# Kernel optimization log

Hardware: AMD Instinct MI355X
Metric: run time of the kernel (lower is better)

## Reference

```python
import jax, jax.numpy as jnp
import numpy as np

B, S, D, H = 2, 2048, 1024, 16
HD = D // H  # head dim = 64


def setup_inputs() -> dict:
    key = jax.random.key(0)
    ks = jax.random.split(key, 8)
    s = 0.02
    return {
        "Q": jax.random.normal(ks[0], (B, S, D), jnp.float32),
        "K": jax.random.normal(ks[1], (B, S, D), jnp.float32),
        "V": jax.random.normal(ks[2], (B, S, D), jnp.float32),
        "mask": jax.random.randint(ks[3], (1, 1, S, S), 0, 2, jnp.int32),
        "Wq": jax.random.normal(ks[4], (D, D), jnp.float32) * s,
        "bq": jnp.zeros((D,), jnp.float32),
        "Wk": jax.random.normal(ks[5], (D, D), jnp.float32) * s,
        "bk": jnp.zeros((D,), jnp.float32),
        "Wv": jax.random.normal(ks[6], (D, D), jnp.float32) * s,
        "bv": jnp.zeros((D,), jnp.float32),
        "Wo": jax.random.normal(ks[7], (D, D), jnp.float32) * s,
        "bo": jnp.zeros((D,), jnp.float32),
    }


def reference(Q, K, V, mask, Wq, bq, Wk, bk, Wv, bv, Wo, bo):
    b = Q.shape[0]
    # QKV projections, split into heads: [B,S,D] -> [B,H,S,HD]
    q = (Q @ Wq + bq).reshape(b, -1, H, HD).transpose(0, 2, 1, 3)
    k = (K @ Wk + bk).reshape(b, -1, H, HD).transpose(0, 2, 1, 3)
    v = (V @ Wv + bv).reshape(b, -1, H, HD).transpose(0, 2, 1, 3)
    # scaled dot-product attention with full [B,H,S,S] scores (as in source)
    scale = jnp.sqrt(jnp.asarray(HD, q.dtype))
    scores = jnp.einsum("bhqd,bhkd->bhqk", q, k) / scale
    scores = jnp.where(mask == 0, -jnp.inf, scores)
    attn = jax.nn.softmax(scores, axis=-1)
    ctx = jnp.einsum("bhqk,bhkd->bhqd", attn, v)
    # merge heads and output projection
    concat = ctx.transpose(0, 2, 1, 3).reshape(b, -1, H * HD)
    return concat @ Wo + bo
```

## Files before the change

### kernel.cpp

```cpp
#include <hip/hip_runtime.h>


using s8v = __attribute__((ext_vector_type(8))) short;
using f4v = __attribute__((ext_vector_type(4))) float;
using f16v = __attribute__((ext_vector_type(16))) float;
typedef unsigned long long u64;

__device__ __forceinline__ unsigned short f2bf(float f) {
  union { float f; unsigned int u; } v; v.f = f;
  return (unsigned short)((v.u + 0x7fffu + ((v.u >> 16) & 1u)) >> 16);
}

__device__ __forceinline__ unsigned pkbf(float lo, float hi2) {
  return __builtin_amdgcn_perm(__float_as_uint(hi2), __float_as_uint(lo), 0x07060302);
}

__device__ __forceinline__ void gll16(const void* g, void* l) {
  __builtin_amdgcn_global_load_lds(
      (const __attribute__((address_space(1))) unsigned int*)g,
      (__attribute__((address_space(3))) unsigned int*)l, 16, 0, 0);
}

__global__ void prep_kernel(const float* __restrict__ Q, const float* __restrict__ K,
                            const float* __restrict__ V,
                            unsigned short* __restrict__ qb, unsigned short* __restrict__ kb,
                            unsigned short* __restrict__ vb,
                            const float* __restrict__ W0, const float* __restrict__ W1,
                            const float* __restrict__ W2, const float* __restrict__ W3,
                            unsigned short* __restrict__ T0, unsigned short* __restrict__ T1,
                            unsigned short* __restrict__ T2, unsigned short* __restrict__ T3,
                            const int* __restrict__ mask, unsigned* __restrict__ bmw) {
  __shared__ unsigned short t[64][72];
  const int bid = blockIdx.x, tid = threadIdx.x;
  if (bid < 12288) {
    int z = bid >> 12;
    int idx = (bid & 4095) * 256 + tid;
    const float* in = (z == 0) ? Q : (z == 1) ? K : V;
    unsigned short* out = (z == 0) ? qb : (z == 1) ? kb : vb;
    float4 v = ((const float4*)in)[idx];
    ushort4 o;
    o.x = f2bf(v.x); o.y = f2bf(v.y); o.z = f2bf(v.z); o.w = f2bf(v.w);
    ((ushort4*)out)[idx] = o;
  } else if (bid < 13312) {
    int b = bid - 12288;
    int z = b >> 8, rem = b & 255;
    int k0 = (rem >> 4) * 64, n0 = (rem & 15) * 64;
    const float* W = (z == 0) ? W0 : (z == 1) ? W1 : (z == 2) ? W2 : W3;
    unsigned short* Wt = (z == 0) ? T0 : (z == 1) ? T1 : (z == 2) ? T2 : T3;
    for (int p = 0; p < 4; ++p) {
      int idx = p * 256 + tid;
      int row = idx >> 4, c4 = idx & 15;
      float4 v = *(const float4*)&W[(size_t)(k0 + row) * 1024 + n0 + c4 * 4];
      t[row][c4 * 4 + 0] = f2bf(v.x);
      t[row][c4 * 4 + 1] = f2bf(v.y);
      t[row][c4 * 4 + 2] = f2bf(v.z);
      t[row][c4 * 4 + 3] = f2bf(v.w);
    }
    __syncthreads();
    for (int p = 0; p < 2; ++p) {
      int idx = p * 256 + tid;
      int j = idx >> 3, c8 = idx & 7;
      unsigned short tmp[8];
      for (int i = 0; i < 8; ++i) tmp[i] = t[c8 * 8 + i][j];
      uint4 o;
      o.x = tmp[0] | ((unsigned)tmp[1] << 16);
      o.y = tmp[2] | ((unsigned)tmp[3] << 16);
      o.z = tmp[4] | ((unsigned)tmp[5] << 16);
      o.w = tmp[6] | ((unsigned)tmp[7] << 16);
      *(uint4*)&Wt[(size_t)(n0 + j) * 1024 + k0 + c8 * 8] = o;
    }
  } else {
    int g = (bid - 13312) * 256 + tid;
    int widx = g & 15, hi = (g >> 4) & 1, l31 = (g >> 5) & 31;
    int it = (g >> 10) & 31, rowblk = g >> 15;
    int ni = widx >> 3, kcl = (widx >> 2) & 1, e = widx & 3;
    int kk = 64 * it + 32 * ni + 16 * kcl + 4 * hi + (e >> 1) * 8 + (e & 1) * 2;
    int qrow = rowblk * 32 + l31;
    const int* mrow = mask + (size_t)qrow * 2048 + kk;
    unsigned wd = (mrow[0] ? 0xFFFFu : 0u) | (mrow[1] ? 0xFFFF0000u : 0u);
    bmw[g] = wd;
  }
}

__global__ __launch_bounds__(256) void proj3_kernel(
    const unsigned short* __restrict__ A0, const unsigned short* __restrict__ A1,
    const unsigned short* __restrict__ A2,
    const unsigned short* __restrict__ W0, const unsigned short* __restrict__ W1,
    const unsigned short* __restrict__ W2,
    const float* __restrict__ b0, const float* __restrict__ b1, const float* __restrict__ b2,
    unsigned short* __restrict__ oq, unsigned short* __restrict__ ok,
    unsigned short* __restrict__ ovt) {
  const int z = blockIdx.z;
  const unsigned short* A  = (z == 0) ? A0 : (z == 1) ? A1 : A2;
  const unsigned short* Wt = (z == 0) ? W0 : (z == 1) ? W1 : W2;
  const float* bias        = (z == 0) ? b0 : (z == 1) ? b1 : b2;

  __shared__ __align__(16) unsigned short As[64 * 32];
  __shared__ __align__(16) unsigned short Bs[128 * 32];

  const int tid = threadIdx.x;
  const int lane = tid & 63, w = tid >> 6, ln = lane & 15, quad = lane >> 4;
  const int wm = (w & 1) * 32, wn = (w >> 1) * 64;
  const int m0 = blockIdx.x * 64, n0 = blockIdx.y * 128;

  const int slr = lane >> 2;
  const int schunk = (lane & 3) ^ ((lane >> 3) & 3);
  const int cfrag = (quad ^ ((ln >> 1) & 3)) * 8;

  f4v zero = {0.f, 0.f, 0.f, 0.f};
  f4v acc[2][4];
  for (int mi = 0; mi < 2; ++mi)
    for (int ni = 0; ni < 4; ++ni) acc[mi][ni] = zero;

  for (int kt = 0; kt < 1024; kt += 32) {
    __syncthreads();
    gll16(&A[(size_t)(m0 + w * 16 + slr) * 1024 + kt + schunk * 8],        &As[(w * 16) * 32]);
    gll16(&Wt[(size_t)(n0 + w * 32 + slr) * 1024 + kt + schunk * 8],       &Bs[(w * 32) * 32]);
    gll16(&Wt[(size_t)(n0 + w * 32 + 16 + slr) * 1024 + kt + schunk * 8],  &Bs[(w * 32 + 16) * 32]);
    __syncthreads();
    s8v a[2], b[4];
    for (int mi = 0; mi < 2; ++mi) a[mi] = *(const s8v*)&As[(wm + mi * 16 + ln) * 32 + cfrag];
    for (int ni = 0; ni < 4; ++ni) b[ni] = *(const s8v*)&Bs[(wn + ni * 16 + ln) * 32 + cfrag];
    if (z < 2) {
      for (int mi = 0; mi < 2; ++mi)
        for (int ni = 0; ni < 4; ++ni)
          acc[mi][ni] = __builtin_amdgcn_mfma_f32_16x16x32_bf16(a[mi], b[ni], acc[mi][ni], 0, 0, 0);
    } else {
      for (int mi = 0; mi < 2; ++mi)
        for (int ni = 0; ni < 4; ++ni)
          acc[mi][ni] = __builtin_amdgcn_mfma_f32_16x16x32_bf16(b[ni], a[mi], acc[mi][ni], 0, 0, 0);
    }
  }

  if (z < 2) {
    const float qscale = (z == 0) ? 0.18033688f : 1.0f;
    unsigned short* outp = (z == 0) ? oq : ok;
    for (int mi = 0; mi < 2; ++mi) {
      int rb = m0 + wm + mi * 16 + quad * 4;
      int b_ = rb >> 11;
      for (int ni = 0; ni < 4; ++ni) {
        int col = n0 + wn + ni * 16 + ln;
        float bvv = bias[col];
        int h = col >> 6, hd = col & 63;
        size_t ob = (size_t)(b_ * 16 + h) * 2048;
        for (int r = 0; r < 4; ++r) {
          int s = (rb + r) & 2047;
          outp[(ob + s) * 64 + hd] = f2bf((acc[mi][ni][r] + bvv) * qscale);
        }
      }
    }
  } else {
    for (int ni = 0; ni < 4; ++ni) {
      for (int r = 0; r < 4; ++r) {
        int colw = n0 + wn + ni * 16 + quad * 4 + r;
        int h = colw >> 6, hd = colw & 63;
        float bvv = bias[colw];
        for (int mi = 0; mi < 2; ++mi) {
          int sg = m0 + wm + mi * 16 + ln;
          int b_ = sg >> 11, ss = sg & 2047;
          ovt[((size_t)(b_ * 16 + h) * 64 + hd) * 2048 + ss] = f2bf(acc[mi][ni][r] + bvv);
        }
      }
    }
  }
}

__global__ __launch_bounds__(256, 2) void flash_kernel(
    const unsigned short* __restrict__ q, const unsigned short* __restrict__ k,
    const unsigned short* __restrict__ vt, const unsigned* __restrict__ bmw,
    unsigned short* __restrict__ ctx) {
  __shared__ __align__(16) unsigned short k_s[2][64][72];
  __shared__ __align__(16) unsigned short v_s[2][64][72];

  const int tid = threadIdx.x;
  const int lane = tid & 63, w = tid >> 6;
  const int l31 = lane & 31, hi = lane >> 5;
  const int q0 = blockIdx.x * 128;
  const int bh = blockIdx.y;
  const unsigned short* qg  = q  + ((size_t)bh * 2048 + q0) * 64;
  const unsigned short* kgb = k  + (size_t)bh * 2048 * 64;
  const unsigned short* vgb = vt + (size_t)bh * 64 * 2048;
  const unsigned* mwp = bmw + (size_t)(blockIdx.x * 4 + w) * 32768 + l31 * 32 + hi * 16;

  const int qrow = w * 32 + l31;
  s8v qf[4];
#pragma unroll
  for (int c = 0; c < 4; ++c)
    qf[c] = *(const s8v*)&qg[(size_t)qrow * 64 + c * 16 + hi * 8];

  s8v ones;
#pragma unroll
  for (int i = 0; i < 8; ++i) ones[i] = (short)0x3F80;
  f16v zf;
#pragma unroll
  for (int i = 0; i < 16; ++i) zf[i] = 0.f;

  const int srow = tid >> 3, sc8 = tid & 7;

  uint4 kr0 = *(const uint4*)&kgb[(size_t)srow * 64 + sc8 * 8];
  uint4 kr1 = *(const uint4*)&kgb[(size_t)(srow + 32) * 64 + sc8 * 8];
  uint4 vr0 = *(const uint4*)&vgb[(size_t)srow * 2048 + sc8 * 8];
  uint4 vr1 = *(const uint4*)&vgb[(size_t)(srow + 32) * 2048 + sc8 * 8];
  *(uint4*)&k_s[0][srow][sc8 * 8] = kr0;
  *(uint4*)&k_s[0][srow + 32][sc8 * 8] = kr1;
  *(uint4*)&v_s[0][srow][sc8 * 8] = vr0;
  *(uint4*)&v_s[0][srow + 32][sc8 * 8] = vr1;
  kr0 = *(const uint4*)&kgb[(size_t)(64 + srow) * 64 + sc8 * 8];
  kr1 = *(const uint4*)&kgb[(size_t)(64 + srow + 32) * 64 + sc8 * 8];
  vr0 = *(const uint4*)&vgb[(size_t)srow * 2048 + 64 + sc8 * 8];
  vr1 = *(const uint4*)&vgb[(size_t)(srow + 32) * 2048 + 64 + sc8 * 8];
  __syncthreads();

  f16v o0, o1, lac;
#pragma unroll
  for (int i = 0; i < 16; ++i) { o0[i] = 0.f; o1[i] = 0.f; lac[i] = 0.f; }

  for (int kt = 0; kt < 2048; kt += 64) {
    const int cur = (kt >> 6) & 1;
    const uint4* mw4 = (const uint4*)(mwp + (kt >> 6) * 1024);
    const uint4 mwA = mw4[0], mwB = mw4[1], mwC = mw4[2], mwD = mw4[3];

    if (kt + 64 < 2048) {
      const int nxt = cur ^ 1;
      *(uint4*)&k_s[nxt][srow][sc8 * 8] = kr0;
      *(uint4*)&k_s[nxt][srow + 32][sc8 * 8] = kr1;
      *(uint4*)&v_s[nxt][srow][sc8 * 8] = vr0;
      *(uint4*)&v_s[nxt][srow + 32][sc8 * 8] = vr1;
      if (kt + 128 < 2048) {
        const int kn = kt + 128;
        kr0 = *(const uint4*)&kgb[(size_t)(kn + srow) * 64 + sc8 * 8];
        kr1 = *(const uint4*)&kgb[(size_t)(kn + srow + 32) * 64 + sc8 * 8];
        vr0 = *(const uint4*)&vgb[(size_t)srow * 2048 + kn + sc8 * 8];
        vr1 = *(const uint4*)&vgb[(size_t)(srow + 32) * 2048 + kn + sc8 * 8];
      }
    }

    __builtin_amdgcn_s_setprio(1);
    s8v ak0 = *(const s8v*)&k_s[cur][l31][hi * 8];
    s8v ak1 = *(const s8v*)&k_s[cur][32 + l31][hi * 8];
    f16v s0 = __builtin_amdgcn_mfma_f32_32x32x16_bf16(ak0, qf[0], zf, 0, 0, 0);
    f16v s1 = __builtin_amdgcn_mfma_f32_32x32x16_bf16(ak1, qf[0], zf, 0, 0, 0);
#pragma unroll
    for (int c = 1; c < 4; ++c) {
      ak0 = *(const s8v*)&k_s[cur][l31][c * 16 + hi * 8];
      ak1 = *(const s8v*)&k_s[cur][32 + l31][c * 16 + hi * 8];
      s0 = __builtin_amdgcn_mfma_f32_32x32x16_bf16(ak0, qf[c], s0, 0, 0, 0);
      s1 = __builtin_amdgcn_mfma_f32_32x32x16_bf16(ak1, qf[c], s1, 0, 0, 0);
    }
    __builtin_amdgcn_s_setprio(0);

    s8v pf[4];
#pragma unroll
    for (int ni = 0; ni < 2; ++ni) {
      float p[16];
#pragma unroll
      for (int i = 0; i < 16; ++i)
        p[i] = __builtin_amdgcn_exp2f(ni ? s1[i] : s0[i]);
#pragma unroll
      for (int kcl = 0; kcl < 2; ++kcl) {
        const int rb = 8 * kcl;
        const uint4 mw = ni ? (kcl ? mwD : mwC) : (kcl ? mwB : mwA);
        unsigned x0 = pkbf(p[rb + 0], p[rb + 1]) & mw.x;
        unsigned x1 = pkbf(p[rb + 2], p[rb + 3]) & mw.y;
        unsigned y0 = pkbf(p[rb + 4], p[rb + 5]) & mw.z;
        unsigned y1 = pkbf(p[rb + 6], p[rb + 7]) & mw.w;
        asm("v_permlane32_swap_b32 %0, %1" : "+v"(x0), "+v"(y0));
        asm("v_permlane32_swap_b32 %0, %1" : "+v"(x1), "+v"(y1));
        union { uint4 u; s8v v; } cv;
        cv.u = make_uint4(x0, x1, y0, y1);
        pf[ni * 2 + kcl] = cv.v;
      }
    }

    __builtin_amdgcn_s_setprio(1);
#pragma unroll
    for (int kc = 0; kc < 4; ++kc)
      lac = __builtin_amdgcn_mfma_f32_32x32x16_bf16(pf[kc], ones, lac, 0, 0, 0);
#pragma unroll
    for (int kc = 0; kc < 4; ++kc) {
      s8v bv0 = *(const s8v*)&v_s[cur][l31][kc * 16 + hi * 8];
      s8v bv1 = *(const s8v*)&v_s[cur][32 + l31][kc * 16 + hi * 8];
      o0 = __builtin_amdgcn_mfma_f32_32x32x16_bf16(pf[kc], bv0, o0, 0, 0, 0);
      o1 = __builtin_amdgcn_mfma_f32_32x32x16_bf16(pf[kc], bv1, o1, 0, 0, 0);
    }
    __builtin_amdgcn_s_setprio(0);
    __syncthreads();
  }

  const int b_ = bh >> 4, h = bh & 15;
#pragma unroll
  for (int r = 0; r < 16; ++r) {
    const int ql = (r & 3) + 8 * (r >> 2) + 4 * hi;
    const float inv = 1.f / lac[r];
    const int srw = q0 + w * 32 + ql;
    const size_t base = ((size_t)b_ * 2048 + srw) * 1024 + h * 64;
    ctx[base + l31] = f2bf(o0[r] * inv);
    ctx[base + 32 + l31] = f2bf(o1[r] * inv);
  }
}

__global__ __launch_bounds__(256) void gemm_out_kernel(
    const unsigned short* __restrict__ A, const unsigned short* __restrict__ Wt,
    const float* __restrict__ bias, float* __restrict__ out) {
  __shared__ __align__(16) unsigned short As[64 * 32];
  __shared__ __align__(16) unsigned short Bs[128 * 32];

  const int tid = threadIdx.x;
  const int lane = tid & 63, w = tid >> 6, ln = lane & 15, quad = lane >> 4;
  const int wm = (w & 1) * 32, wn = (w >> 1) * 64;
  const int m0 = blockIdx.x * 64, n0 = blockIdx.y * 128;

  const int slr = lane >> 2;
  const int schunk = (lane & 3) ^ ((lane >> 3) & 3);
  const int cfrag = (quad ^ ((ln >> 1) & 3)) * 8;

  f4v zero = {0.f, 0.f, 0.f, 0.f};
  f4v acc[2][4];
  for (int mi = 0; mi < 2; ++mi)
    for (int ni = 0; ni < 4; ++ni) acc[mi][ni] = zero;

  for (int kt = 0; kt < 1024; kt += 32) {
    __syncthreads();
    gll16(&A[(size_t)(m0 + w * 16 + slr) * 1024 + kt + schunk * 8],        &As[(w * 16) * 32]);
    gll16(&Wt[(size_t)(n0 + w * 32 + slr) * 1024 + kt + schunk * 8],       &Bs[(w * 32) * 32]);
    gll16(&Wt[(size_t)(n0 + w * 32 + 16 + slr) * 1024 + kt + schunk * 8],  &Bs[(w * 32 + 16) * 32]);
    __syncthreads();
    s8v a[2], b[4];
    for (int mi = 0; mi < 2; ++mi) a[mi] = *(const s8v*)&As[(wm + mi * 16 + ln) * 32 + cfrag];
    for (int ni = 0; ni < 4; ++ni) b[ni] = *(const s8v*)&Bs[(wn + ni * 16 + ln) * 32 + cfrag];
    for (int mi = 0; mi < 2; ++mi)
      for (int ni = 0; ni < 4; ++ni)
        acc[mi][ni] = __builtin_amdgcn_mfma_f32_16x16x32_bf16(a[mi], b[ni], acc[mi][ni], 0, 0, 0);
  }

  for (int mi = 0; mi < 2; ++mi) {
    int rb = m0 + wm + mi * 16 + quad * 4;
    for (int ni = 0; ni < 4; ++ni) {
      int col = n0 + wn + ni * 16 + ln;
      float bvv = bias[col];
      for (int r = 0; r < 4; ++r)
        out[(size_t)(rb + r) * 1024 + col] = acc[mi][ni][r] + bvv;
    }
  }
}

extern "C" void kernel_launch(void* const* d_in, const int* in_sizes, int n_in,
                              void* d_out, int out_size, void* d_ws, size_t ws_size,
                              hipStream_t stream) {
  const float* Q  = (const float*)d_in[0];
  const float* K  = (const float*)d_in[1];
  const float* V  = (const float*)d_in[2];
  const int* mask = (const int*)d_in[3];
  const float* Wq = (const float*)d_in[4];
  const float* bq = (const float*)d_in[5];
  const float* Wk = (const float*)d_in[6];
  const float* bk = (const float*)d_in[7];
  const float* Wv = (const float*)d_in[8];
  const float* bv = (const float*)d_in[9];
  const float* Wo = (const float*)d_in[10];
  const float* bo = (const float*)d_in[11];
  float* out = (float*)d_out;

  char* ws = (char*)d_ws;
  const size_t MB = 1u << 20;
  unsigned short* qb  = (unsigned short*)(ws + 0 * MB);
  unsigned short* kb  = (unsigned short*)(ws + 8 * MB);
  unsigned short* vb  = (unsigned short*)(ws + 16 * MB);
  unsigned short* wqt = (unsigned short*)(ws + 24 * MB);
  unsigned short* wkt = (unsigned short*)(ws + 26 * MB);
  unsigned short* wvt = (unsigned short*)(ws + 28 * MB);
  unsigned short* wot = (unsigned short*)(ws + 30 * MB);
  unsigned short* qh  = (unsigned short*)(ws + 32 * MB);
  unsigned short* kh  = (unsigned short*)(ws + 40 * MB);
  unsigned short* vth = (unsigned short*)(ws + 48 * MB);
  unsigned* bmw       = (unsigned*)(ws + 56 * MB);
  unsigned short* ctx = (unsigned short*)(ws + 16 * MB);

  prep_kernel<<<21504, 256, 0, stream>>>(Q, K, V, qb, kb, vb,
                                         Wq, Wk, Wv, Wo, wqt, wkt, wvt, wot,
                                         mask, bmw);
  proj3_kernel<<<dim3(64, 8, 3), 256, 0, stream>>>(qb, kb, vb, wqt, wkt, wvt,
                                                   bq, bk, bv, qh, kh, vth);
  flash_kernel<<<dim3(16, 32), 256, 0, stream>>>(qh, kh, vth, bmw, ctx);
  gemm_out_kernel<<<dim3(64, 8), 256, 0, stream>>>(ctx, wot, bo, out);
}
```

Measured before the change: 247.3 us.

## Split flash attention KV range across warp pairs with 64-row query blocks

Each flash block now handles 64 query rows instead of 128. Its four waves form two groups, and each group processes half of the key range, one taking the first 1024 keys and the other the last 1024, using both LDS buffers at the same time. The partial outputs and row sums are combined through shared memory before normalisation. The grid doubles to 1024 blocks and the launch bounds ask for 3 blocks per CU, to improve occupancy and load balance across the GPU's CUs. In exchange, the double-buffer overlap now needs two barriers per iteration and there is an extra reduction step at the end.

New measurement: 265.2 us. +7.2%, slower.

```diff
diff --git a/kernel.cpp b/kernel.cpp
--- a/kernel.cpp
+++ b/kernel.cpp
@@ -165,7 +165,7 @@
   }
 }
 
-__global__ __launch_bounds__(256, 2) void flash_kernel(
+__global__ __launch_bounds__(256, 3) void flash_kernel(
     const unsigned short* __restrict__ q, const unsigned short* __restrict__ k,
     const unsigned short* __restrict__ vt, const unsigned* __restrict__ bmw,
     unsigned short* __restrict__ ctx) {
@@ -175,14 +175,17 @@
   const int tid = threadIdx.x;
   const int lane = tid & 63, w = tid >> 6;
   const int l31 = lane & 31, hi = lane >> 5;
-  const int q0 = blockIdx.x * 128;
+  const int h = w & 1;
+  const int g = w >> 1;
+  const int q0 = blockIdx.x * 64;
   const int bh = blockIdx.y;
   const unsigned short* qg  = q  + ((size_t)bh * 2048 + q0) * 64;
   const unsigned short* kgb = k  + (size_t)bh * 2048 * 64;
   const unsigned short* vgb = vt + (size_t)bh * 64 * 2048;
-  const unsigned* mwp = bmw + (size_t)(blockIdx.x * 4 + w) * 32768 + l31 * 32 + hi * 16;
-
-  const int qrow = w * 32 + l31;
+  const unsigned* mwp = bmw + ((size_t)(blockIdx.x * 2 + g) * 32 + h * 16) * 1024
+                        + l31 * 32 + hi * 16;
+
+  const int qrow = g * 32 + l31;
   s8v qf[4];
 #pragma unroll
   for (int c = 0; c < 4; ++c)
@@ -197,53 +200,51 @@
 
   const int srow = tid >> 3, sc8 = tid & 7;
 
-  uint4 kr0 = *(const uint4*)&kgb[(size_t)srow * 64 + sc8 * 8];
-  uint4 kr1 = *(const uint4*)&kgb[(size_t)(srow + 32) * 64 + sc8 * 8];
-  uint4 vr0 = *(const uint4*)&vgb[(size_t)srow * 2048 + sc8 * 8];
-  uint4 vr1 = *(const uint4*)&vgb[(size_t)(srow + 32) * 2048 + sc8 * 8];
-  *(uint4*)&k_s[0][srow][sc8 * 8] = kr0;
-  *(uint4*)&k_s[0][srow + 32][sc8 * 8] = kr1;
-  *(uint4*)&v_s[0][srow][sc8 * 8] = vr0;
-  *(uint4*)&v_s[0][srow + 32][sc8 * 8] = vr1;
-  kr0 = *(const uint4*)&kgb[(size_t)(64 + srow) * 64 + sc8 * 8];
-  kr1 = *(const uint4*)&kgb[(size_t)(64 + srow + 32) * 64 + sc8 * 8];
-  vr0 = *(const uint4*)&vgb[(size_t)srow * 2048 + 64 + sc8 * 8];
-  vr1 = *(const uint4*)&vgb[(size_t)(srow + 32) * 2048 + 64 + sc8 * 8];
+  uint4 ka0, ka1, kb0, kb1, va0, va1, vb0, vb1;
+  auto LOADT = [&](int it) {
+    const int kA = it * 64, kB = 1024 + it * 64;
+    ka0 = *(const uint4*)&kgb[(size_t)(kA + srow) * 64 + sc8 * 8];
+    ka1 = *(const uint4*)&kgb[(size_t)(kA + srow + 32) * 64 + sc8 * 8];
+    kb0 = *(const uint4*)&kgb[(size_t)(kB + srow) * 64 + sc8 * 8];
+    kb1 = *(const uint4*)&kgb[(size_t)(kB + srow + 32) * 64 + sc8 * 8];
+    va0 = *(const uint4*)&vgb[(size_t)srow * 2048 + kA + sc8 * 8];
+    va1 = *(const uint4*)&vgb[(size_t)(srow + 32) * 2048 + kA + sc8 * 8];
+    vb0 = *(const uint4*)&vgb[(size_t)srow * 2048 + kB + sc8 * 8];
+    vb1 = *(const uint4*)&vgb[(size_t)(srow + 32) * 2048 + kB + sc8 * 8];
+  };
+  auto WRITET = [&]() {
+    *(uint4*)&k_s[0][srow][sc8 * 8] = ka0;
+    *(uint4*)&k_s[0][srow + 32][sc8 * 8] = ka1;
+    *(uint4*)&k_s[1][srow][sc8 * 8] = kb0;
+    *(uint4*)&k_s[1][srow + 32][sc8 * 8] = kb1;
+    *(uint4*)&v_s[0][srow][sc8 * 8] = va0;
+    *(uint4*)&v_s[0][srow + 32][sc8 * 8] = va1;
+    *(uint4*)&v_s[1][srow][sc8 * 8] = vb0;
+    *(uint4*)&v_s[1][srow + 32][sc8 * 8] = vb1;
+  };
+
+  LOADT(0);
+  WRITET();
+  LOADT(1);
   __syncthreads();
 
   f16v o0, o1, lac;
 #pragma unroll
   for (int i = 0; i < 16; ++i) { o0[i] = 0.f; o1[i] = 0.f; lac[i] = 0.f; }
 
-  for (int kt = 0; kt < 2048; kt += 64) {
-    const int cur = (kt >> 6) & 1;
-    const uint4* mw4 = (const uint4*)(mwp + (kt >> 6) * 1024);
+  for (int i = 0; i < 16; ++i) {
+    const uint4* mw4 = (const uint4*)(mwp + i * 1024);
     const uint4 mwA = mw4[0], mwB = mw4[1], mwC = mw4[2], mwD = mw4[3];
 
-    if (kt + 64 < 2048) {
-      const int nxt = cur ^ 1;
-      *(uint4*)&k_s[nxt][srow][sc8 * 8] = kr0;
-      *(uint4*)&k_s[nxt][srow + 32][sc8 * 8] = kr1;
-      *(uint4*)&v_s[nxt][srow][sc8 * 8] = vr0;
-      *(uint4*)&v_s[nxt][srow + 32][sc8 * 8] = vr1;
-      if (kt + 128 < 2048) {
-        const int kn = kt + 128;
-        kr0 = *(const uint4*)&kgb[(size_t)(kn + srow) * 64 + sc8 * 8];
-        kr1 = *(const uint4*)&kgb[(size_t)(kn + srow + 32) * 64 + sc8 * 8];
-        vr0 = *(const uint4*)&vgb[(size_t)srow * 2048 + kn + sc8 * 8];
-        vr1 = *(const uint4*)&vgb[(size_t)(srow + 32) * 2048 + kn + sc8 * 8];
-      }
-    }
-
     __builtin_amdgcn_s_setprio(1);
-    s8v ak0 = *(const s8v*)&k_s[cur][l31][hi * 8];
-    s8v ak1 = *(const s8v*)&k_s[cur][32 + l31][hi * 8];
+    s8v ak0 = *(const s8v*)&k_s[h][l31][hi * 8];
+    s8v ak1 = *(const s8v*)&k_s[h][32 + l31][hi * 8];
     f16v s0 = __builtin_amdgcn_mfma_f32_32x32x16_bf16(ak0, qf[0], zf, 0, 0, 0);
     f16v s1 = __builtin_amdgcn_mfma_f32_32x32x16_bf16(ak1, qf[0], zf, 0, 0, 0);
 #pragma unroll
     for (int c = 1; c < 4; ++c) {
-      ak0 = *(const s8v*)&k_s[cur][l31][c * 16 + hi * 8];
-      ak1 = *(const s8v*)&k_s[cur][32 + l31][c * 16 + hi * 8];
+      ak0 = *(const s8v*)&k_s[h][l31][c * 16 + hi * 8];
+      ak1 = *(const s8v*)&k_s[h][32 + l31][c * 16 + hi * 8];
       s0 = __builtin_amdgcn_mfma_f32_32x32x16_bf16(ak0, qf[c], s0, 0, 0, 0);
       s1 = __builtin_amdgcn_mfma_f32_32x32x16_bf16(ak1, qf[c], s1, 0, 0, 0);
     }
@@ -254,8 +255,8 @@
     for (int ni = 0; ni < 2; ++ni) {
       float p[16];
 #pragma unroll
-      for (int i = 0; i < 16; ++i)
-        p[i] = __builtin_amdgcn_exp2f(ni ? s1[i] : s0[i]);
+      for (int i2 = 0; i2 < 16; ++i2)
+        p[i2] = __builtin_amdgcn_exp2f(ni ? s1[i2] : s0[i2]);
 #pragma unroll
       for (int kcl = 0; kcl < 2; ++kcl) {
         const int rb = 8 * kcl;
@@ -278,24 +279,43 @@
       lac = __builtin_amdgcn_mfma_f32_32x32x16_bf16(pf[kc], ones, lac, 0, 0, 0);
 #pragma unroll
     for (int kc = 0; kc < 4; ++kc) {
-      s8v bv0 = *(const s8v*)&v_s[cur][l31][kc * 16 + hi * 8];
-      s8v bv1 = *(const s8v*)&v_s[cur][32 + l31][kc * 16 + hi * 8];
+      s8v bv0 = *(const s8v*)&v_s[h][l31][kc * 16 + hi * 8];
+      s8v bv1 = *(const s8v*)&v_s[h][32 + l31][kc * 16 + hi * 8];
       o0 = __builtin_amdgcn_mfma_f32_32x32x16_bf16(pf[kc], bv0, o0, 0, 0, 0);
       o1 = __builtin_amdgcn_mfma_f32_32x32x16_bf16(pf[kc], bv1, o1, 0, 0, 0);
     }
     __builtin_amdgcn_s_setprio(0);
-    __syncthreads();
-  }
-
-  const int b_ = bh >> 4, h = bh & 15;
-#pragma unroll
-  for (int r = 0; r < 16; ++r) {
-    const int ql = (r & 3) + 8 * (r >> 2) + 4 * hi;
-    const float inv = 1.f / lac[r];
-    const int srw = q0 + w * 32 + ql;
-    const size_t base = ((size_t)b_ * 2048 + srw) * 1024 + h * 64;
-    ctx[base + l31] = f2bf(o0[r] * inv);
-    ctx[base + 32 + l31] = f2bf(o1[r] * inv);
+
+    __syncthreads();
+    if (i < 15) WRITET();
+    if (i < 14) LOADT(i + 2);
+    __syncthreads();
+  }
+
+  float* cb = g ? (float*)&v_s[0][0][0] : (float*)&k_s[0][0][0];
+  if (h == 1) {
+#pragma unroll
+    for (int r = 0; r < 16; r += 4) {
+      *(float4*)&cb[lane * 52 + r]      = make_float4(o0[r], o0[r+1], o0[r+2], o0[r+3]);
+      *(float4*)&cb[lane * 52 + 16 + r] = make_float4(o1[r], o1[r+1], o1[r+2], o1[r+3]);
+      *(float4*)&cb[lane * 52 + 32 + r] = make_float4(lac[r], lac[r+1], lac[r+2], lac[r+3]);
+    }
+  }
+  __syncthreads();
+  if (h == 0) {
+    const int b_ = bh >> 4, hh = bh & 15;
+#pragma unroll
+    for (int r = 0; r < 16; ++r) {
+      const float oo0 = o0[r] + cb[lane * 52 + r];
+      const float oo1 = o1[r] + cb[lane * 52 + 16 + r];
+      const float ll  = lac[r] + cb[lane * 52 + 32 + r];
+      const float inv = 1.f / ll;
+      const int ql = (r & 3) + 8 * (r >> 2) + 4 * hi;
+      const int srw = q0 + g * 32 + ql;
+      const size_t base = ((size_t)b_ * 2048 + srw) * 1024 + hh * 64;
+      ctx[base + l31] = f2bf(oo0 * inv);
+      ctx[base + 32 + l31] = f2bf(oo1 * inv);
+    }
   }
 }
 
@@ -381,6 +401,6 @@
                                          mask, bmw);
   proj3_kernel<<<dim3(64, 8, 3), 256, 0, stream>>>(qb, kb, vb, wqt, wkt, wvt,
                                                    bq, bk, bv, qh, kh, vth);
-  flash_kernel<<<dim3(16, 32), 256, 0, stream>>>(qh, kh, vth, bmw, ctx);
+  flash_kernel<<<dim3(32, 32), 256, 0, stream>>>(qh, kh, vth, bmw, ctx);
   gemm_out_kernel<<<dim3(64, 8), 256, 0, stream>>>(ctx, wot, bo, out);
 }
```

## Software-pipeline QK^T of the next tile with softmax and PV of the current

Applied to the files above, without the earlier changes.

Restructures the flash attention loop so the QK^T MFMAs for tile i+1 are issued before the exp/pack and PV MFMAs of tile i, with the score registers ping-ponged through a two-way manually unrolled macro. This lets matrix-core work overlap the exp and permute VALU work. The mask words for the next tile are prefetched one iteration ahead, and the global-to-LDS staging is rescheduled with two barriers per iteration. It raises register pressure with two live score sets, which may hurt occupancy under launch_bounds(256,2).

New measurement: 246.1 us. About the same (-0.5%).

```diff
diff --git a/kernel.cpp b/kernel.cpp
--- a/kernel.cpp
+++ b/kernel.cpp
@@ -165,6 +165,74 @@
   }
 }
 
+#define FLASH_ITER(i, SIN0, SIN1, SOUT0, SOUT1)                                 \
+  {                                                                             \
+    const int cur = (i) & 1;                                                    \
+    uint4 nA, nB, nC, nD;                                                       \
+    if ((i) < 31) {                                                             \
+      const uint4* m4 = (const uint4*)(mwp + ((i) + 1) * 1024);                 \
+      nA = m4[0]; nB = m4[1]; nC = m4[2]; nD = m4[3];                           \
+    }                                                                           \
+          \
+    __builtin_amdgcn_s_setprio(1);                                              \
+    if ((i) < 31) {                                                             \
+      s8v ak0 = *(const s8v*)&k_s[cur ^ 1][l31][hi * 8];                        \
+      s8v ak1 = *(const s8v*)&k_s[cur ^ 1][32 + l31][hi * 8];                   \
+      SOUT0 = __builtin_amdgcn_mfma_f32_32x32x16_bf16(ak0, qf[0], zf, 0, 0, 0); \
+      SOUT1 = __builtin_amdgcn_mfma_f32_32x32x16_bf16(ak1, qf[0], zf, 0, 0, 0); \
+      _Pragma("unroll")                                                         \
+      for (int c = 1; c < 4; ++c) {                                             \
+        ak0 = *(const s8v*)&k_s[cur ^ 1][l31][c * 16 + hi * 8];                 \
+        ak1 = *(const s8v*)&k_s[cur ^ 1][32 + l31][c * 16 + hi * 8];            \
+        SOUT0 = __builtin_amdgcn_mfma_f32_32x32x16_bf16(ak0, qf[c], SOUT0, 0, 0, 0); \
+        SOUT1 = __builtin_amdgcn_mfma_f32_32x32x16_bf16(ak1, qf[c], SOUT1, 0, 0, 0); \
+      }                                                                         \
+    }                                                                           \
+    __builtin_amdgcn_s_setprio(0);                                              \
+         \
+    s8v pf[4];                                                                  \
+    _Pragma("unroll")                                                           \
+    for (int ni = 0; ni < 2; ++ni) {                                            \
+      const f16v sv = ni ? SIN1 : SIN0;                                         \
+      _Pragma("unroll")                                                         \
+      for (int kcl = 0; kcl < 2; ++kcl) {                                       \
+        const int rb = 8 * kcl;                                                 \
+        const uint4 mw = ni ? (kcl ? mwD : mwC) : (kcl ? mwB : mwA);            \
+        unsigned x0 = pkbf(__builtin_amdgcn_exp2f(sv[rb + 0]),                  \
+                           __builtin_amdgcn_exp2f(sv[rb + 1])) & mw.x;          \
+        unsigned x1 = pkbf(__builtin_amdgcn_exp2f(sv[rb + 2]),                  \
+                           __builtin_amdgcn_exp2f(sv[rb + 3])) & mw.y;          \
+        unsigned y0 = pkbf(__builtin_amdgcn_exp2f(sv[rb + 4]),                  \
+                           __builtin_amdgcn_exp2f(sv[rb + 5])) & mw.z;          \
+        unsigned y1 = pkbf(__builtin_amdgcn_exp2f(sv[rb + 6]),                  \
+                           __builtin_amdgcn_exp2f(sv[rb + 7])) & mw.w;          \
+        asm("v_permlane32_swap_b32 %0, %1" : "+v"(x0), "+v"(y0));               \
+        asm("v_permlane32_swap_b32 %0, %1" : "+v"(x1), "+v"(y1));               \
+        union { uint4 u; s8v v; } cv;                                           \
+        cv.u = make_uint4(x0, x1, y0, y1);                                      \
+        pf[ni * 2 + kcl] = cv.v;                                                \
+      }                                                                         \
+    }                                                                           \
+                                              \
+    __builtin_amdgcn_s_setprio(1);                                              \
+    _Pragma("unroll")                                                           \
+    for (int kc = 0; kc < 4; ++kc)                                              \
+      lac = __builtin_amdgcn_mfma_f32_32x32x16_bf16(pf[kc], ones, lac, 0, 0, 0);\
+    _Pragma("unroll")                                                           \
+    for (int kc = 0; kc < 4; ++kc) {                                            \
+      s8v bv0 = *(const s8v*)&v_s[cur][l31][kc * 16 + hi * 8];                  \
+      s8v bv1 = *(const s8v*)&v_s[cur][32 + l31][kc * 16 + hi * 8];             \
+      o0 = __builtin_amdgcn_mfma_f32_32x32x16_bf16(pf[kc], bv0, o0, 0, 0, 0);   \
+      o1 = __builtin_amdgcn_mfma_f32_32x32x16_bf16(pf[kc], bv1, o1, 0, 0, 0);   \
+    }                                                                           \
+    __builtin_amdgcn_s_setprio(0);                                              \
+    __syncthreads();                             \
+    if ((i) < 30) WRITET(cur);                         \
+    if ((i) < 29) LOADT((i) + 3);                                               \
+    __syncthreads();                      \
+    mwA = nA; mwB = nB; mwC = nC; mwD = nD;                                     \
+  }
+
 __global__ __launch_bounds__(256, 2) void flash_kernel(
     const unsigned short* __restrict__ q, const unsigned short* __restrict__ k,
     const unsigned short* __restrict__ vt, const unsigned* __restrict__ bmw,
@@ -197,94 +265,55 @@
 
   const int srow = tid >> 3, sc8 = tid & 7;
 
-  uint4 kr0 = *(const uint4*)&kgb[(size_t)srow * 64 + sc8 * 8];
-  uint4 kr1 = *(const uint4*)&kgb[(size_t)(srow + 32) * 64 + sc8 * 8];
-  uint4 vr0 = *(const uint4*)&vgb[(size_t)srow * 2048 + sc8 * 8];
-  uint4 vr1 = *(const uint4*)&vgb[(size_t)(srow + 32) * 2048 + sc8 * 8];
-  *(uint4*)&k_s[0][srow][sc8 * 8] = kr0;
-  *(uint4*)&k_s[0][srow + 32][sc8 * 8] = kr1;
-  *(uint4*)&v_s[0][srow][sc8 * 8] = vr0;
-  *(uint4*)&v_s[0][srow + 32][sc8 * 8] = vr1;
-  kr0 = *(const uint4*)&kgb[(size_t)(64 + srow) * 64 + sc8 * 8];
-  kr1 = *(const uint4*)&kgb[(size_t)(64 + srow + 32) * 64 + sc8 * 8];
-  vr0 = *(const uint4*)&vgb[(size_t)srow * 2048 + 64 + sc8 * 8];
-  vr1 = *(const uint4*)&vgb[(size_t)(srow + 32) * 2048 + 64 + sc8 * 8];
+  uint4 kr0, kr1, vr0, vr1;
+  auto LOADT = [&](int it) {
+    const int kk = it * 64;
+    kr0 = *(const uint4*)&kgb[(size_t)(kk + srow) * 64 + sc8 * 8];
+    kr1 = *(const uint4*)&kgb[(size_t)(kk + srow + 32) * 64 + sc8 * 8];
+    vr0 = *(const uint4*)&vgb[(size_t)srow * 2048 + kk + sc8 * 8];
+    vr1 = *(const uint4*)&vgb[(size_t)(srow + 32) * 2048 + kk + sc8 * 8];
+  };
+  auto WRITET = [&](int b) {
+    *(uint4*)&k_s[b][srow][sc8 * 8] = kr0;
+    *(uint4*)&k_s[b][srow + 32][sc8 * 8] = kr1;
+    *(uint4*)&v_s[b][srow][sc8 * 8] = vr0;
+    *(uint4*)&v_s[b][srow + 32][sc8 * 8] = vr1;
+  };
+
+  LOADT(0); WRITET(0);
+  LOADT(1); WRITET(1);
+  LOADT(2);
   __syncthreads();
 
+  uint4 mwA, mwB, mwC, mwD;
+  {
+    const uint4* m4 = (const uint4*)mwp;
+    mwA = m4[0]; mwB = m4[1]; mwC = m4[2]; mwD = m4[3];
+  }
+
+  f16v sA0, sA1, sB0, sB1;
+  {
+    s8v ak0 = *(const s8v*)&k_s[0][l31][hi * 8];
+    s8v ak1 = *(const s8v*)&k_s[0][32 + l31][hi * 8];
+    sA0 = __builtin_amdgcn_mfma_f32_32x32x16_bf16(ak0, qf[0], zf, 0, 0, 0);
+    sA1 = __builtin_amdgcn_mfma_f32_32x32x16_bf16(ak1, qf[0], zf, 0, 0, 0);
+#pragma unroll
+    for (int c = 1; c < 4; ++c) {
+      ak0 = *(const s8v*)&k_s[0][l31][c * 16 + hi * 8];
+      ak1 = *(const s8v*)&k_s[0][32 + l31][c * 16 + hi * 8];
+      sA0 = __builtin_amdgcn_mfma_f32_32x32x16_bf16(ak0, qf[c], sA0, 0, 0, 0);
+      sA1 = __builtin_amdgcn_mfma_f32_32x32x16_bf16(ak1, qf[c], sA1, 0, 0, 0);
+    }
+  }
+
   f16v o0, o1, lac;
 #pragma unroll
   for (int i = 0; i < 16; ++i) { o0[i] = 0.f; o1[i] = 0.f; lac[i] = 0.f; }
 
-  for (int kt = 0; kt < 2048; kt += 64) {
-    const int cur = (kt >> 6) & 1;
-    const uint4* mw4 = (const uint4*)(mwp + (kt >> 6) * 1024);
-    const uint4 mwA = mw4[0], mwB = mw4[1], mwC = mw4[2], mwD = mw4[3];
-
-    if (kt + 64 < 2048) {
-      const int nxt = cur ^ 1;
-      *(uint4*)&k_s[nxt][srow][sc8 * 8] = kr0;
-      *(uint4*)&k_s[nxt][srow + 32][sc8 * 8] = kr1;
-      *(uint4*)&v_s[nxt][srow][sc8 * 8] = vr0;
-      *(uint4*)&v_s[nxt][srow + 32][sc8 * 8] = vr1;
-      if (kt + 128 < 2048) {
-        const int kn = kt + 128;
-        kr0 = *(const uint4*)&kgb[(size_t)(kn + srow) * 64 + sc8 * 8];
-        kr1 = *(const uint4*)&kgb[(size_t)(kn + srow + 32) * 64 + sc8 * 8];
-        vr0 = *(const uint4*)&vgb[(size_t)srow * 2048 + kn + sc8 * 8];
-        vr1 = *(const uint4*)&vgb[(size_t)(srow + 32) * 2048 + kn + sc8 * 8];
-      }
-    }
-
-    __builtin_amdgcn_s_setprio(1);
-    s8v ak0 = *(const s8v*)&k_s[cur][l31][hi * 8];
-    s8v ak1 = *(const s8v*)&k_s[cur][32 + l31][hi * 8];
-    f16v s0 = __builtin_amdgcn_mfma_f32_32x32x16_bf16(ak0, qf[0], zf, 0, 0, 0);
-    f16v s1 = __builtin_amdgcn_mfma_f32_32x32x16_bf16(ak1, qf[0], zf, 0, 0, 0);
-#pragma unroll
-    for (int c = 1; c < 4; ++c) {
-      ak0 = *(const s8v*)&k_s[cur][l31][c * 16 + hi * 8];
-      ak1 = *(const s8v*)&k_s[cur][32 + l31][c * 16 + hi * 8];
-      s0 = __builtin_amdgcn_mfma_f32_32x32x16_bf16(ak0, qf[c], s0, 0, 0, 0);
-      s1 = __builtin_amdgcn_mfma_f32_32x32x16_bf16(ak1, qf[c], s1, 0, 0, 0);
-    }
-    __builtin_amdgcn_s_setprio(0);
-
-    s8v pf[4];
-#pragma unroll
-    for (int ni = 0; ni < 2; ++ni) {
-      float p[16];
-#pragma unroll
-      for (int i = 0; i < 16; ++i)
-        p[i] = __builtin_amdgcn_exp2f(ni ? s1[i] : s0[i]);
-#pragma unroll
-      for (int kcl = 0; kcl < 2; ++kcl) {
-        const int rb = 8 * kcl;
-        const uint4 mw = ni ? (kcl ? mwD : mwC) : (kcl ? mwB : mwA);
-        unsigned x0 = pkbf(p[rb + 0], p[rb + 1]) & mw.x;
-        unsigned x1 = pkbf(p[rb + 2], p[rb + 3]) & mw.y;
-        unsigned y0 = pkbf(p[rb + 4], p[rb + 5]) & mw.z;
-        unsigned y1 = pkbf(p[rb + 6], p[rb + 7]) & mw.w;
-        asm("v_permlane32_swap_b32 %0, %1" : "+v"(x0), "+v"(y0));
-        asm("v_permlane32_swap_b32 %0, %1" : "+v"(x1), "+v"(y1));
-        union { uint4 u; s8v v; } cv;
-        cv.u = make_uint4(x0, x1, y0, y1);
-        pf[ni * 2 + kcl] = cv.v;
-      }
-    }
-
-    __builtin_amdgcn_s_setprio(1);
-#pragma unroll
-    for (int kc = 0; kc < 4; ++kc)
-      lac = __builtin_amdgcn_mfma_f32_32x32x16_bf16(pf[kc], ones, lac, 0, 0, 0);
-#pragma unroll
-    for (int kc = 0; kc < 4; ++kc) {
-      s8v bv0 = *(const s8v*)&v_s[cur][l31][kc * 16 + hi * 8];
-      s8v bv1 = *(const s8v*)&v_s[cur][32 + l31][kc * 16 + hi * 8];
-      o0 = __builtin_amdgcn_mfma_f32_32x32x16_bf16(pf[kc], bv0, o0, 0, 0, 0);
-      o1 = __builtin_amdgcn_mfma_f32_32x32x16_bf16(pf[kc], bv1, o1, 0, 0, 0);
-    }
-    __builtin_amdgcn_s_setprio(0);
-    __syncthreads();
+  for (int ii = 0; ii < 16; ++ii) {
+    const int i0 = ii * 2;
+    FLASH_ITER(i0,     sA0, sA1, sB0, sB1);
+    FLASH_ITER(i0 + 1, sB0, sB1, sA0, sA1);
   }
 
   const int b_ = bh >> 4, h = bh & 15;
```
